# Performance work log

Hardware: AMD Instinct MI355X
Metric: run time of the kernel (lower is better)

## Reference

```python
import jax, jax.numpy as jnp
import numpy as np
from jax import lax

B, T, F = 4096, 100, 40
H_ENC, H_LAT, H_DEC = 64, 32, 64


def _lstm(x, Wih, Whh, b):
    """PyTorch-convention LSTM (gate order i,f,g,o), batch_first, zero init state.
    x: [B,T,Fin], Wih: [4H,Fin], Whh: [4H,H], b: [4H] (= b_ih + b_hh).
    Returns hidden sequence [B,T,H]."""
    H = Whh.shape[1]
    # precompute input contributions for all timesteps in one GEMM
    xg = jnp.einsum('btf,gf->btg', x, Wih) + b  # [B,T,4H]
    h0 = jnp.zeros((x.shape[0], H), dtype=x.dtype)
    c0 = jnp.zeros((x.shape[0], H), dtype=x.dtype)

    def step(carry, gx_t):
        h, c = carry
        gates = gx_t + h @ Whh.T  # [B,4H]
        i, f, g, o = jnp.split(gates, 4, axis=-1)
        c = jax.nn.sigmoid(f) * c + jax.nn.sigmoid(i) * jnp.tanh(g)
        h = jax.nn.sigmoid(o) * jnp.tanh(c)
        return (h, c), h

    _, hs = lax.scan(step, (h0, c0), jnp.swapaxes(xg, 0, 1))  # [T,B,H]
    return jnp.swapaxes(hs, 0, 1)


def setup_inputs() -> dict:
    key = jax.random.key(0)
    ks = jax.random.split(key, 8)
    s = 0.05
    return {
        'x': jax.random.normal(ks[0], (B, T, F), dtype=jnp.float32),
        'enc_Wih': jax.random.normal(ks[1], (4 * H_ENC, F), dtype=jnp.float32) * s,
        'enc_Whh': jax.random.normal(ks[2], (4 * H_ENC, H_ENC), dtype=jnp.float32) * s,
        'enc_b': jnp.zeros((4 * H_ENC,), dtype=jnp.float32),
        'lat_Wih': jax.random.normal(ks[3], (4 * H_LAT, H_ENC), dtype=jnp.float32) * s,
        'lat_Whh': jax.random.normal(ks[4], (4 * H_LAT, H_LAT), dtype=jnp.float32) * s,
        'lat_b': jnp.zeros((4 * H_LAT,), dtype=jnp.float32),
        'dec_Wih': jax.random.normal(ks[5], (4 * H_DEC, H_LAT), dtype=jnp.float32) * s,
        'dec_Whh': jax.random.normal(ks[6], (4 * H_DEC, H_DEC), dtype=jnp.float32) * s,
        'dec_b': jnp.zeros((4 * H_DEC,), dtype=jnp.float32),
        'out_W': jax.random.normal(ks[7], (F, H_DEC), dtype=jnp.float32) * s,
        'out_b': jnp.zeros((F,), dtype=jnp.float32),
    }


def reference(x, enc_Wih, enc_Whh, enc_b, lat_Wih, lat_Whh, lat_b,
              dec_Wih, dec_Whh, dec_b, out_W, out_b):
    h = _lstm(x, enc_Wih, enc_Whh, enc_b)                 # [B,T,64]
    last = h[:, -1:, :]                                   # [B,1,64]
    rep = jnp.broadcast_to(last, (h.shape[0], h.shape[1], last.shape[-1]))
    h = _lstm(rep, lat_Wih, lat_Whh, lat_b)               # [B,T,32]
    h = _lstm(h, dec_Wih, dec_Whh, dec_b)                 # [B,T,64]
    return jnp.einsum('bth,fh->btf', h, out_W) + out_b    # [B,T,40]
```

## Files before the change

kernel.cpp:

```cpp
#include <hip/hip_runtime.h>
#include <cstddef>

typedef __attribute__((ext_vector_type(8))) short bf16x8;
typedef __attribute__((ext_vector_type(4))) float f32x4;

#define MFMA(a, b, c) __builtin_amdgcn_mfma_f32_16x16x32_bf16((a), (b), (c), 0, 0, 0)

static __device__ __forceinline__ unsigned hi_bits(float f) {
  unsigned u = __builtin_bit_cast(unsigned, f);
  return (u + 0x8000u) & 0xFFFF0000u;
}
static __device__ __forceinline__ float asf(unsigned u) {
  return __builtin_bit_cast(float, u);
}
static __device__ __forceinline__ unsigned pack_hi(unsigned a, unsigned b) {
  return __builtin_amdgcn_perm(b, a, 0x07060302u);
}
static __device__ __forceinline__ unsigned short f2bf(float f) {
  unsigned u = __builtin_bit_cast(unsigned, f);
  u = u + 0x7FFFu + ((u >> 16) & 1u);
  return (unsigned short)(u >> 16);
}
static __device__ __forceinline__ float bf2f(unsigned short h) {
  unsigned u = ((unsigned)h) << 16;
  return __builtin_bit_cast(float, u);
}
static __device__ __forceinline__ float fast_sig(float x) {
  return __builtin_amdgcn_rcpf(1.0f + __expf(-x));
}
static __device__ __forceinline__ float fast_tanh(float x) {
  return 2.0f * __builtin_amdgcn_rcpf(1.0f + __expf(-2.0f * x)) - 1.0f;
}

static __device__ __forceinline__ void lds_barrier() {
  asm volatile("s_waitcnt lgkmcnt(0)\n\ts_barrier" ::: "memory");
}

static __device__ __forceinline__ bf16x8 aread(const char* base, int lane, int kc) {
  int b = lane & 15, g = lane >> 4;
  int off = (kc * 64 + g * 16) ^ ((b & 7) << 4);
  return *(const bf16x8*)(base + b * 256 + off);
}
static __device__ __forceinline__ void awrite16(char* base, int b, int k, unsigned short v) {
  int off = (2 * k) ^ ((b & 7) << 4);
  *(unsigned short*)(base + b * 256 + off) = v;
}
static __device__ __forceinline__ void awrite32(char* base, int b, int k, unsigned v) {
  int off = (2 * k) ^ ((b & 7) << 4);
  *(unsigned*)(base + b * 256 + off) = v;
}

extern "C" __global__ __launch_bounds__(512, 2)
void lstm_ae_mfma7(const float* __restrict__ x,
                   const float* __restrict__ eWih, const float* __restrict__ eWhh, const float* __restrict__ eb,
                   const float* __restrict__ lWih, const float* __restrict__ lWhh, const float* __restrict__ lb,
                   const float* __restrict__ dWih, const float* __restrict__ dWhh, const float* __restrict__ db,
                   const float* __restrict__ oW,  const float* __restrict__ ob,
                   float* __restrict__ out)
{
  __shared__ __align__(16) char sAhi[2][4096];
  __shared__ __align__(16) char sAlo[2][4096];

  const int tid  = threadIdx.x;
  const int lane = tid & 63;
  const int w    = tid >> 6;
  const int c16  = lane & 15;
  const int p4   = lane >> 4;
  const int bbase = blockIdx.x * 16;

  {
    f32x4 z = {0.f, 0.f, 0.f, 0.f};
    *(f32x4*)(&sAhi[0][0] + tid * 16) = z;
    *(f32x4*)(&sAlo[0][0] + tid * 16) = z;
  }

  bf16x8 ewh[2][4], ewl[2][4];
  float ebias[2][4];
#pragma unroll
  for (int n = 0; n < 2; ++n) {
    int tr = c16;
    int u = w * 8 + (tr >> 2) * 2 + n;
    int ga = tr & 3;
#pragma unroll
    for (int r = 0; r < 4; ++r) ebias[n][r] = eb[r * 64 + (w * 8 + p4 * 2 + n)];
#pragma unroll
    for (int kc = 0; kc < 4; ++kc) {
      bf16x8 hi, lo;
#pragma unroll
      for (int e = 0; e < 8; ++e) {
        int k = kc * 32 + p4 * 8 + e;
        float v = 0.f;
        if (k < 40)       v = eWih[(ga * 64 + u) * 40 + k];
        else if (k >= 64) v = eWhh[(ga * 64 + u) * 64 + (k - 64)];
        unsigned short hh = f2bf(v);
        hi[e] = (short)hh;
        lo[e] = (short)f2bf(v - bf2f(hh));
      }
      ewh[n][kc] = hi; ewl[n][kc] = lo;
    }
  }

  lds_barrier();

  if (tid < 160) {
    int b = tid / 10, f4 = tid - b * 10;
    f32x4 ld = *(const f32x4*)(x + ((size_t)(bbase + b) * 100 + 0) * 40 + f4 * 4);
    unsigned xh[4], xl[4];
#pragma unroll
    for (int e = 0; e < 4; ++e) {
      xh[e] = hi_bits(ld[e]);
      xl[e] = __builtin_bit_cast(unsigned, ld[e] - asf(xh[e]));
    }
    unsigned long long ph = (unsigned long long)pack_hi(xh[0], xh[1])
                          | ((unsigned long long)pack_hi(xh[2], xh[3]) << 32);
    unsigned long long pl = (unsigned long long)pack_hi(xl[0], xl[1])
                          | ((unsigned long long)pack_hi(xl[2], xl[3]) << 32);
    int off = (f4 * 8) ^ ((b & 7) << 4);
    *(unsigned long long*)(sAhi[0] + b * 256 + off) = ph;
    *(unsigned long long*)(sAlo[0] + b * 256 + off) = pl;
  }

  float cE[2] = {0.f, 0.f};
  int q = 0;
  lds_barrier();

#pragma unroll 1
  for (int t = 0; t < 100; ++t) {
    f32x4 xld;
    int sb = 0, sf4 = 0;
    const bool stager = (tid < 160);
    if (stager) {
      int tn = (t + 1 < 100) ? t + 1 : 99;
      sb = tid / 10; sf4 = tid - sb * 10;
      xld = *(const f32x4*)(x + ((size_t)(bbase + sb) * 100 + tn) * 40 + sf4 * 4);
    }

    f32x4 acc[2], acc2[2];
#pragma unroll
    for (int n = 0; n < 2; ++n) {
      acc[n]  = f32x4{ebias[n][0], ebias[n][1], ebias[n][2], ebias[n][3]};
      acc2[n] = f32x4{0.f, 0.f, 0.f, 0.f};
    }
    const char* Ah = sAhi[q];
    const char* Al = sAlo[q];
    __builtin_amdgcn_s_setprio(1);
#pragma unroll
    for (int kc = 0; kc < 4; ++kc) {
      bf16x8 ah = aread(Ah, lane, kc);
      bf16x8 al = aread(Al, lane, kc);
#pragma unroll
      for (int n = 0; n < 2; ++n) {
        f32x4 t0 = (kc < 2) ? acc[n] : acc2[n];
        t0 = MFMA(ewh[n][kc], ah, t0);
        t0 = MFMA(ewl[n][kc], ah, t0);
        t0 = MFMA(ewh[n][kc], al, t0);
        if (kc < 2) acc[n] = t0; else acc2[n] = t0;
      }
    }
    __builtin_amdgcn_s_setprio(0);

    char* AhN = sAhi[q ^ 1];
    char* AlN = sAlo[q ^ 1];
    unsigned hhb[2], hlb[2];
#pragma unroll
    for (int n = 0; n < 2; ++n) {
      f32x4 gv = acc[n] + acc2[n];
      float ii = fast_sig(gv[0]), ff = fast_sig(gv[1]);
      float gg = fast_tanh(gv[2]), oo = fast_sig(gv[3]);
      cE[n] = ff * cE[n] + ii * gg;
      float hv = oo * fast_tanh(cE[n]);
      hhb[n] = hi_bits(hv);
      hlb[n] = __builtin_bit_cast(unsigned, hv - asf(hhb[n]));
    }
    awrite32(AhN, c16, 64 + w * 8 + p4 * 2, pack_hi(hhb[0], hhb[1]));
    awrite32(AlN, c16, 64 + w * 8 + p4 * 2, pack_hi(hlb[0], hlb[1]));

    if (stager) {
      unsigned xh[4], xl[4];
#pragma unroll
      for (int e = 0; e < 4; ++e) {
        xh[e] = hi_bits(xld[e]);
        xl[e] = __builtin_bit_cast(unsigned, xld[e] - asf(xh[e]));
      }
      unsigned long long ph = (unsigned long long)pack_hi(xh[0], xh[1])
                            | ((unsigned long long)pack_hi(xh[2], xh[3]) << 32);
      unsigned long long pl = (unsigned long long)pack_hi(xl[0], xl[1])
                            | ((unsigned long long)pack_hi(xl[2], xl[3]) << 32);
      int off = (sf4 * 8) ^ ((sb & 7) << 4);
      *(unsigned long long*)(AhN + sb * 256 + off) = ph;
      *(unsigned long long*)(AlN + sb * 256 + off) = pl;
    }
    lds_barrier();
    q ^= 1;
  }

  f32x4 xga;
  {
    int tr = c16;
    int u = w * 4 + (tr >> 2), ga = tr & 3;
    int ul = w * 4 + p4;
    xga = f32x4{lb[ul], lb[32 + ul], lb[64 + ul], lb[96 + ul]};
#pragma unroll
    for (int kci = 0; kci < 2; ++kci) {
      bf16x8 hi, lo;
#pragma unroll
      for (int e = 0; e < 8; ++e) {
        float v = lWih[(ga * 32 + u) * 64 + kci * 32 + p4 * 8 + e];
        unsigned short hh = f2bf(v);
        hi[e] = (short)hh;
        lo[e] = (short)f2bf(v - bf2f(hh));
      }
      bf16x8 ah = aread(sAhi[q], lane, 2 + kci);
      bf16x8 al = aread(sAlo[q], lane, 2 + kci);
      xga = MFMA(hi, ah, xga);
      xga = MFMA(lo, ah, xga);
      xga = MFMA(hi, al, xga);
    }
  }
  lds_barrier();

  {
    f32x4 z = {0.f, 0.f, 0.f, 0.f};
    *(f32x4*)(&sAhi[0][0] + tid * 16) = z;
    *(f32x4*)(&sAlo[0][0] + tid * 16) = z;
  }

  bf16x8 lwh, lwl;
  {
    int tr = c16;
    int u = w * 4 + (tr >> 2), ga = tr & 3;
    bf16x8 hi, lo;
#pragma unroll
    for (int e = 0; e < 8; ++e) {
      float v = lWhh[(ga * 32 + u) * 32 + p4 * 8 + e];
      unsigned short hh = f2bf(v);
      hi[e] = (short)hh;
      lo[e] = (short)f2bf(v - bf2f(hh));
    }
    lwh = hi; lwl = lo;
  }
  bf16x8 dwh[2][3], dwl[2][3];
  float dbias[2][4];
#pragma unroll
  for (int n = 0; n < 2; ++n) {
    int tr = c16;
    int u = w * 8 + (tr >> 2) * 2 + n;
    int ga = tr & 3;
#pragma unroll
    for (int r = 0; r < 4; ++r) dbias[n][r] = db[r * 64 + (w * 8 + p4 * 2 + n)];
#pragma unroll
    for (int kc = 0; kc < 3; ++kc) {
      bf16x8 hi, lo;
#pragma unroll
      for (int e = 0; e < 8; ++e) {
        int k = kc * 32 + p4 * 8 + e;
        float v = (k < 32) ? dWih[(ga * 64 + u) * 32 + k]
                           : dWhh[(ga * 64 + u) * 64 + (k - 32)];
        unsigned short hh = f2bf(v);
        hi[e] = (short)hh;
        lo[e] = (short)f2bf(v - bf2f(hh));
      }
      dwh[n][kc] = hi; dwl[n][kc] = lo;
    }
  }
  bf16x8 pwh[2], pwl[2];
  float pbias[4];
#pragma unroll
  for (int r = 0; r < 4; ++r) {
    int f = w * 16 + p4 * 4 + r;
    pbias[r] = (w < 3 && f < 40) ? ob[f] : 0.0f;
  }
  if (w < 3) {
    int f = w * 16 + c16;
#pragma unroll
    for (int kci = 0; kci < 2; ++kci) {
      bf16x8 hi, lo;
#pragma unroll
      for (int e = 0; e < 8; ++e) {
        float v = (f < 40) ? oW[f * 64 + kci * 32 + p4 * 8 + e] : 0.0f;
        unsigned short hh = f2bf(v);
        hi[e] = (short)hh;
        lo[e] = (short)f2bf(v - bf2f(hh));
      }
      pwh[kci] = hi; pwl[kci] = lo;
    }
  }

  float cL = 0.f;
  float cD[2] = {0.f, 0.f};
  lds_barrier();

#pragma unroll 1
  for (int i = 0; i < 102; ++i) {
    const int pa = i & 1;
    bf16x8 c0h = aread(sAhi[pa ^ 1], lane, 0), c0l = aread(sAlo[pa ^ 1], lane, 0);
    bf16x8 d1h = aread(sAhi[pa], lane, 1),     d1l = aread(sAlo[pa], lane, 1);
    bf16x8 d2h = aread(sAhi[pa], lane, 2),     d2l = aread(sAlo[pa], lane, 2);

    if (i < 100) {
      __builtin_amdgcn_s_setprio(1);
      f32x4 lac = xga;
      lac = MFMA(lwh, c0h, lac);
      lac = MFMA(lwl, c0h, lac);
      lac = MFMA(lwh, c0l, lac);
      __builtin_amdgcn_s_setprio(0);
      float ii = fast_sig(lac[0]), ff = fast_sig(lac[1]);
      float gg = fast_tanh(lac[2]), oo = fast_sig(lac[3]);
      cL = ff * cL + ii * gg;
      float hv = oo * fast_tanh(cL);
      unsigned hb = hi_bits(hv);
      float lov = hv - asf(hb);
      awrite16(sAhi[pa], c16, w * 4 + p4, (unsigned short)(hb >> 16));
      awrite16(sAlo[pa], c16, w * 4 + p4,
               (unsigned short)(__builtin_bit_cast(unsigned, lov) >> 16));
    }

    if (i >= 1 && i < 101) {
      unsigned hhb[2], hlb[2];
#pragma unroll
      for (int n = 0; n < 2; ++n) {
        f32x4 dac = f32x4{dbias[n][0], dbias[n][1], dbias[n][2], dbias[n][3]};
        __builtin_amdgcn_s_setprio(1);
        dac = MFMA(dwh[n][0], c0h, dac);
        dac = MFMA(dwl[n][0], c0h, dac);
        dac = MFMA(dwh[n][0], c0l, dac);
        dac = MFMA(dwh[n][1], d1h, dac);
        dac = MFMA(dwl[n][1], d1h, dac);
        dac = MFMA(dwh[n][1], d1l, dac);
        dac = MFMA(dwh[n][2], d2h, dac);
        dac = MFMA(dwl[n][2], d2h, dac);
        dac = MFMA(dwh[n][2], d2l, dac);
        __builtin_amdgcn_s_setprio(0);
        float ii = fast_sig(dac[0]), ff = fast_sig(dac[1]);
        float gg = fast_tanh(dac[2]), oo = fast_sig(dac[3]);
        cD[n] = ff * cD[n] + ii * gg;
        float hv = oo * fast_tanh(cD[n]);
        hhb[n] = hi_bits(hv);
        hlb[n] = __builtin_bit_cast(unsigned, hv - asf(hhb[n]));
      }
      awrite32(sAhi[pa ^ 1], c16, 32 + w * 8 + p4 * 2, pack_hi(hhb[0], hhb[1]));
      awrite32(sAlo[pa ^ 1], c16, 32 + w * 8 + p4 * 2, pack_hi(hlb[0], hlb[1]));
    }

    if (i >= 2 && w < 3) {
      f32x4 pac = f32x4{pbias[0], pbias[1], pbias[2], pbias[3]};
      __builtin_amdgcn_s_setprio(1);
      pac = MFMA(pwh[0], d1h, pac);
      pac = MFMA(pwl[0], d1h, pac);
      pac = MFMA(pwh[0], d1l, pac);
      pac = MFMA(pwh[1], d2h, pac);
      pac = MFMA(pwl[1], d2h, pac);
      pac = MFMA(pwh[1], d2l, pac);
      __builtin_amdgcn_s_setprio(0);
#pragma unroll
      for (int r = 0; r < 4; ++r) {
        int f = w * 16 + p4 * 4 + r;
        if (f < 40)
          out[((size_t)(bbase + c16) * 100 + (i - 2)) * 40 + f] = pac[r];
      }
    }
    lds_barrier();
  }
}

extern "C" void kernel_launch(void* const* d_in, const int* in_sizes, int n_in,
                              void* d_out, int out_size, void* d_ws, size_t ws_size,
                              hipStream_t stream) {
  const float* x    = (const float*)d_in[0];
  const float* eWih = (const float*)d_in[1];
  const float* eWhh = (const float*)d_in[2];
  const float* eb   = (const float*)d_in[3];
  const float* lWih = (const float*)d_in[4];
  const float* lWhh = (const float*)d_in[5];
  const float* lb   = (const float*)d_in[6];
  const float* dWih = (const float*)d_in[7];
  const float* dWhh = (const float*)d_in[8];
  const float* db   = (const float*)d_in[9];
  const float* oW   = (const float*)d_in[10];
  const float* ob   = (const float*)d_in[11];
  float* out = (float*)d_out;

  lstm_ae_mfma7<<<256, 512, 0, stream>>>(x, eWih, eWhh, eb, lWih, lWhh, lb,
                                         dWih, dWhh, db, oW, ob, out);
}
```

Measured before the change: 186.9 us.

## Halve the batch tile per block to four waves and double units per wave

Each block now handles 8 batch rows with 256 threads instead of 16 rows with 512 threads, and the grid doubles to 512 blocks. Each wave computes twice as many gate units per step, so hidden-state writes become 64-bit LDS stores, and the split accumulators and setprio hints are dropped. The aim is smaller barrier groups and two independent blocks per CU that can hide each other's recurrence latency. The cost is that half of each 16-wide MFMA batch dimension now goes unused, which doubles MFMA work per batch row, and each wave's serial dependency chain per step gets longer.

```diff
diff --git a/kernel.cpp b/kernel.cpp
--- a/kernel.cpp
+++ b/kernel.cpp
@@ -41,17 +41,17 @@
   int off = (kc * 64 + g * 16) ^ ((b & 7) << 4);
   return *(const bf16x8*)(base + b * 256 + off);
 }
-static __device__ __forceinline__ void awrite16(char* base, int b, int k, unsigned short v) {
-  int off = (2 * k) ^ ((b & 7) << 4);
-  *(unsigned short*)(base + b * 256 + off) = v;
-}
 static __device__ __forceinline__ void awrite32(char* base, int b, int k, unsigned v) {
   int off = (2 * k) ^ ((b & 7) << 4);
   *(unsigned*)(base + b * 256 + off) = v;
 }
-
-extern "C" __global__ __launch_bounds__(512, 2)
-void lstm_ae_mfma7(const float* __restrict__ x,
+static __device__ __forceinline__ void awrite64(char* base, int b, int k, unsigned long long v) {
+  int off = (2 * k) ^ ((b & 7) << 4);
+  *(unsigned long long*)(base + b * 256 + off) = v;
+}
+
+extern "C" __global__ __launch_bounds__(256, 2)
+void lstm_ae_mfma8(const float* __restrict__ x,
                    const float* __restrict__ eWih, const float* __restrict__ eWhh, const float* __restrict__ eb,
                    const float* __restrict__ lWih, const float* __restrict__ lWhh, const float* __restrict__ lb,
                    const float* __restrict__ dWih, const float* __restrict__ dWhh, const float* __restrict__ db,
@@ -66,23 +66,25 @@
   const int w    = tid >> 6;
   const int c16  = lane & 15;
   const int p4   = lane >> 4;
-  const int bbase = blockIdx.x * 16;
+  const int bbase = blockIdx.x * 8;
 
   {
     f32x4 z = {0.f, 0.f, 0.f, 0.f};
-    *(f32x4*)(&sAhi[0][0] + tid * 16) = z;
-    *(f32x4*)(&sAlo[0][0] + tid * 16) = z;
-  }
-
-  bf16x8 ewh[2][4], ewl[2][4];
-  float ebias[2][4];
-#pragma unroll
-  for (int n = 0; n < 2; ++n) {
-    int tr = c16;
-    int u = w * 8 + (tr >> 2) * 2 + n;
-    int ga = tr & 3;
-#pragma unroll
-    for (int r = 0; r < 4; ++r) ebias[n][r] = eb[r * 64 + (w * 8 + p4 * 2 + n)];
+#pragma unroll
+    for (int i = 0; i < 2; ++i) {
+      *(f32x4*)(&sAhi[0][0] + tid * 16 + i * 4096) = z;
+      *(f32x4*)(&sAlo[0][0] + tid * 16 + i * 4096) = z;
+    }
+  }
+
+  bf16x8 ewh[4][4], ewl[4][4];
+  float ebias[4][4];
+#pragma unroll
+  for (int n = 0; n < 4; ++n) {
+    int u = w * 16 + (c16 >> 2) * 4 + n;
+    int ga = c16 & 3;
+#pragma unroll
+    for (int r = 0; r < 4; ++r) ebias[n][r] = eb[r * 64 + (w * 16 + p4 * 4 + n)];
 #pragma unroll
     for (int kc = 0; kc < 4; ++kc) {
       bf16x8 hi, lo;
@@ -102,9 +104,11 @@
 
   lds_barrier();
 
-  if (tid < 160) {
-    int b = tid / 10, f4 = tid - b * 10;
-    f32x4 ld = *(const f32x4*)(x + ((size_t)(bbase + b) * 100 + 0) * 40 + f4 * 4);
+  const bool stager = (tid >= 176);
+  const int s0 = tid - 176;
+  const int sb = s0 / 10, sf4 = s0 - (s0 / 10) * 10;
+  if (stager) {
+    f32x4 ld = *(const f32x4*)(x + ((size_t)(bbase + sb) * 100 + 0) * 40 + sf4 * 4);
     unsigned xh[4], xl[4];
 #pragma unroll
     for (int e = 0; e < 4; ++e) {
@@ -115,65 +119,61 @@
                           | ((unsigned long long)pack_hi(xh[2], xh[3]) << 32);
     unsigned long long pl = (unsigned long long)pack_hi(xl[0], xl[1])
                           | ((unsigned long long)pack_hi(xl[2], xl[3]) << 32);
-    int off = (f4 * 8) ^ ((b & 7) << 4);
-    *(unsigned long long*)(sAhi[0] + b * 256 + off) = ph;
-    *(unsigned long long*)(sAlo[0] + b * 256 + off) = pl;
-  }
-
-  float cE[2] = {0.f, 0.f};
+    int off = (sf4 * 8) ^ ((sb & 7) << 4);
+    *(unsigned long long*)(sAhi[0] + sb * 256 + off) = ph;
+    *(unsigned long long*)(sAlo[0] + sb * 256 + off) = pl;
+  }
+
+  float cE[4] = {0.f, 0.f, 0.f, 0.f};
   int q = 0;
   lds_barrier();
 
 #pragma unroll 1
   for (int t = 0; t < 100; ++t) {
     f32x4 xld;
-    int sb = 0, sf4 = 0;
-    const bool stager = (tid < 160);
     if (stager) {
       int tn = (t + 1 < 100) ? t + 1 : 99;
-      sb = tid / 10; sf4 = tid - sb * 10;
       xld = *(const f32x4*)(x + ((size_t)(bbase + sb) * 100 + tn) * 40 + sf4 * 4);
     }
 
-    f32x4 acc[2], acc2[2];
-#pragma unroll
-    for (int n = 0; n < 2; ++n) {
-      acc[n]  = f32x4{ebias[n][0], ebias[n][1], ebias[n][2], ebias[n][3]};
-      acc2[n] = f32x4{0.f, 0.f, 0.f, 0.f};
-    }
+    f32x4 acc[4];
+#pragma unroll
+    for (int n = 0; n < 4; ++n)
+      acc[n] = f32x4{ebias[n][0], ebias[n][1], ebias[n][2], ebias[n][3]};
     const char* Ah = sAhi[q];
     const char* Al = sAlo[q];
-    __builtin_amdgcn_s_setprio(1);
 #pragma unroll
     for (int kc = 0; kc < 4; ++kc) {
       bf16x8 ah = aread(Ah, lane, kc);
       bf16x8 al = aread(Al, lane, kc);
 #pragma unroll
-      for (int n = 0; n < 2; ++n) {
-        f32x4 t0 = (kc < 2) ? acc[n] : acc2[n];
-        t0 = MFMA(ewh[n][kc], ah, t0);
-        t0 = MFMA(ewl[n][kc], ah, t0);
-        t0 = MFMA(ewh[n][kc], al, t0);
-        if (kc < 2) acc[n] = t0; else acc2[n] = t0;
-      }
-    }
-    __builtin_amdgcn_s_setprio(0);
+      for (int n = 0; n < 4; ++n) {
+        acc[n] = MFMA(ewh[n][kc], ah, acc[n]);
+        acc[n] = MFMA(ewl[n][kc], ah, acc[n]);
+        acc[n] = MFMA(ewh[n][kc], al, acc[n]);
+      }
+    }
 
     char* AhN = sAhi[q ^ 1];
     char* AlN = sAlo[q ^ 1];
-    unsigned hhb[2], hlb[2];
-#pragma unroll
-    for (int n = 0; n < 2; ++n) {
-      f32x4 gv = acc[n] + acc2[n];
-      float ii = fast_sig(gv[0]), ff = fast_sig(gv[1]);
-      float gg = fast_tanh(gv[2]), oo = fast_sig(gv[3]);
+    unsigned hhb[4], hlb[4];
+#pragma unroll
+    for (int n = 0; n < 4; ++n) {
+      float ii = fast_sig(acc[n][0]), ff = fast_sig(acc[n][1]);
+      float gg = fast_tanh(acc[n][2]), oo = fast_sig(acc[n][3]);
       cE[n] = ff * cE[n] + ii * gg;
       float hv = oo * fast_tanh(cE[n]);
       hhb[n] = hi_bits(hv);
       hlb[n] = __builtin_bit_cast(unsigned, hv - asf(hhb[n]));
     }
-    awrite32(AhN, c16, 64 + w * 8 + p4 * 2, pack_hi(hhb[0], hhb[1]));
-    awrite32(AlN, c16, 64 + w * 8 + p4 * 2, pack_hi(hlb[0], hlb[1]));
+    {
+      unsigned long long ph = (unsigned long long)pack_hi(hhb[0], hhb[1])
+                            | ((unsigned long long)pack_hi(hhb[2], hhb[3]) << 32);
+      unsigned long long pl = (unsigned long long)pack_hi(hlb[0], hlb[1])
+                            | ((unsigned long long)pack_hi(hlb[2], hlb[3]) << 32);
+      awrite64(AhN, c16, 64 + w * 16 + p4 * 4, ph);
+      awrite64(AlN, c16, 64 + w * 16 + p4 * 4, pl);
+    }
 
     if (stager) {
       unsigned xh[4], xl[4];
@@ -194,41 +194,48 @@
     q ^= 1;
   }
 
-  f32x4 xga;
+  f32x4 xga[2];
   {
-    int tr = c16;
-    int u = w * 4 + (tr >> 2), ga = tr & 3;
-    int ul = w * 4 + p4;
-    xga = f32x4{lb[ul], lb[32 + ul], lb[64 + ul], lb[96 + ul]};
-#pragma unroll
-    for (int kci = 0; kci < 2; ++kci) {
-      bf16x8 hi, lo;
-#pragma unroll
-      for (int e = 0; e < 8; ++e) {
-        float v = lWih[(ga * 32 + u) * 64 + kci * 32 + p4 * 8 + e];
-        unsigned short hh = f2bf(v);
-        hi[e] = (short)hh;
-        lo[e] = (short)f2bf(v - bf2f(hh));
-      }
-      bf16x8 ah = aread(sAhi[q], lane, 2 + kci);
-      bf16x8 al = aread(sAlo[q], lane, 2 + kci);
-      xga = MFMA(hi, ah, xga);
-      xga = MFMA(lo, ah, xga);
-      xga = MFMA(hi, al, xga);
+#pragma unroll
+    for (int n = 0; n < 2; ++n) {
+      int u = w * 8 + (c16 >> 2) * 2 + n;
+      int ga = c16 & 3;
+      int ul = w * 8 + p4 * 2 + n;
+      xga[n] = f32x4{lb[ul], lb[32 + ul], lb[64 + ul], lb[96 + ul]};
+#pragma unroll
+      for (int kci = 0; kci < 2; ++kci) {
+        bf16x8 hi, lo;
+#pragma unroll
+        for (int e = 0; e < 8; ++e) {
+          float v = lWih[(ga * 32 + u) * 64 + kci * 32 + p4 * 8 + e];
+          unsigned short hh = f2bf(v);
+          hi[e] = (short)hh;
+          lo[e] = (short)f2bf(v - bf2f(hh));
+        }
+        bf16x8 ah = aread(sAhi[q], lane, 2 + kci);
+        bf16x8 al = aread(sAlo[q], lane, 2 + kci);
+        xga[n] = MFMA(hi, ah, xga[n]);
+        xga[n] = MFMA(lo, ah, xga[n]);
+        xga[n] = MFMA(hi, al, xga[n]);
+      }
     }
   }
   lds_barrier();
 
   {
     f32x4 z = {0.f, 0.f, 0.f, 0.f};
-    *(f32x4*)(&sAhi[0][0] + tid * 16) = z;
-    *(f32x4*)(&sAlo[0][0] + tid * 16) = z;
-  }
-
-  bf16x8 lwh, lwl;
-  {
-    int tr = c16;
-    int u = w * 4 + (tr >> 2), ga = tr & 3;
+#pragma unroll
+    for (int i = 0; i < 2; ++i) {
+      *(f32x4*)(&sAhi[0][0] + tid * 16 + i * 4096) = z;
+      *(f32x4*)(&sAlo[0][0] + tid * 16 + i * 4096) = z;
+    }
+  }
+
+  bf16x8 lwh[2], lwl[2];
+#pragma unroll
+  for (int n = 0; n < 2; ++n) {
+    int u = w * 8 + (c16 >> 2) * 2 + n;
+    int ga = c16 & 3;
     bf16x8 hi, lo;
 #pragma unroll
     for (int e = 0; e < 8; ++e) {
@@ -237,17 +244,16 @@
       hi[e] = (short)hh;
       lo[e] = (short)f2bf(v - bf2f(hh));
     }
-    lwh = hi; lwl = lo;
-  }
-  bf16x8 dwh[2][3], dwl[2][3];
-  float dbias[2][4];
-#pragma unroll
-  for (int n = 0; n < 2; ++n) {
-    int tr = c16;
-    int u = w * 8 + (tr >> 2) * 2 + n;
-    int ga = tr & 3;
-#pragma unroll
-    for (int r = 0; r < 4; ++r) dbias[n][r] = db[r * 64 + (w * 8 + p4 * 2 + n)];
+    lwh[n] = hi; lwl[n] = lo;
+  }
+  bf16x8 dwh[4][3], dwl[4][3];
+  float dbias[4][4];
+#pragma unroll
+  for (int n = 0; n < 4; ++n) {
+    int u = w * 16 + (c16 >> 2) * 4 + n;
+    int ga = c16 & 3;
+#pragma unroll
+    for (int r = 0; r < 4; ++r) dbias[n][r] = db[r * 64 + (w * 16 + p4 * 4 + n)];
 #pragma unroll
     for (int kc = 0; kc < 3; ++kc) {
       bf16x8 hi, lo;
@@ -286,8 +292,8 @@
     }
   }
 
-  float cL = 0.f;
-  float cD[2] = {0.f, 0.f};
+  float cL[2] = {0.f, 0.f};
+  float cD[4] = {0.f, 0.f, 0.f, 0.f};
   lds_barrier();
 
 #pragma unroll 1
@@ -298,29 +304,29 @@
     bf16x8 d2h = aread(sAhi[pa], lane, 2),     d2l = aread(sAlo[pa], lane, 2);
 
     if (i < 100) {
-      __builtin_amdgcn_s_setprio(1);
-      f32x4 lac = xga;
-      lac = MFMA(lwh, c0h, lac);
-      lac = MFMA(lwl, c0h, lac);
-      lac = MFMA(lwh, c0l, lac);
-      __builtin_amdgcn_s_setprio(0);
-      float ii = fast_sig(lac[0]), ff = fast_sig(lac[1]);
-      float gg = fast_tanh(lac[2]), oo = fast_sig(lac[3]);
-      cL = ff * cL + ii * gg;
-      float hv = oo * fast_tanh(cL);
-      unsigned hb = hi_bits(hv);
-      float lov = hv - asf(hb);
-      awrite16(sAhi[pa], c16, w * 4 + p4, (unsigned short)(hb >> 16));
-      awrite16(sAlo[pa], c16, w * 4 + p4,
-               (unsigned short)(__builtin_bit_cast(unsigned, lov) >> 16));
+      unsigned hb[2], lbits[2];
+#pragma unroll
+      for (int n = 0; n < 2; ++n) {
+        f32x4 lac = xga[n];
+        lac = MFMA(lwh[n], c0h, lac);
+        lac = MFMA(lwl[n], c0h, lac);
+        lac = MFMA(lwh[n], c0l, lac);
+        float ii = fast_sig(lac[0]), ff = fast_sig(lac[1]);
+        float gg = fast_tanh(lac[2]), oo = fast_sig(lac[3]);
+        cL[n] = ff * cL[n] + ii * gg;
+        float hv = oo * fast_tanh(cL[n]);
+        hb[n] = hi_bits(hv);
+        lbits[n] = __builtin_bit_cast(unsigned, hv - asf(hb[n]));
+      }
+      awrite32(sAhi[pa], c16, w * 8 + p4 * 2, pack_hi(hb[0], hb[1]));
+      awrite32(sAlo[pa], c16, w * 8 + p4 * 2, pack_hi(lbits[0], lbits[1]));
     }
 
     if (i >= 1 && i < 101) {
-      unsigned hhb[2], hlb[2];
-#pragma unroll
-      for (int n = 0; n < 2; ++n) {
+      unsigned hhb[4], hlb[4];
+#pragma unroll
+      for (int n = 0; n < 4; ++n) {
         f32x4 dac = f32x4{dbias[n][0], dbias[n][1], dbias[n][2], dbias[n][3]};
-        __builtin_amdgcn_s_setprio(1);
         dac = MFMA(dwh[n][0], c0h, dac);
         dac = MFMA(dwl[n][0], c0h, dac);
         dac = MFMA(dwh[n][0], c0l, dac);
@@ -330,7 +336,6 @@
         dac = MFMA(dwh[n][2], d2h, dac);
         dac = MFMA(dwl[n][2], d2h, dac);
         dac = MFMA(dwh[n][2], d2l, dac);
-        __builtin_amdgcn_s_setprio(0);
         float ii = fast_sig(dac[0]), ff = fast_sig(dac[1]);
         float gg = fast_tanh(dac[2]), oo = fast_sig(dac[3]);
         cD[n] = ff * cD[n] + ii * gg;
@@ -338,25 +343,29 @@
         hhb[n] = hi_bits(hv);
         hlb[n] = __builtin_bit_cast(unsigned, hv - asf(hhb[n]));
       }
-      awrite32(sAhi[pa ^ 1], c16, 32 + w * 8 + p4 * 2, pack_hi(hhb[0], hhb[1]));
-      awrite32(sAlo[pa ^ 1], c16, 32 + w * 8 + p4 * 2, pack_hi(hlb[0], hlb[1]));
+      unsigned long long ph = (unsigned long long)pack_hi(hhb[0], hhb[1])
+                            | ((unsigned long long)pack_hi(hhb[2], hhb[3]) << 32);
+      unsigned long long pl = (unsigned long long)pack_hi(hlb[0], hlb[1])
+                            | ((unsigned long long)pack_hi(hlb[2], hlb[3]) << 32);
+      awrite64(sAhi[pa ^ 1], c16, 32 + w * 16 + p4 * 4, ph);
+      awrite64(sAlo[pa ^ 1], c16, 32 + w * 16 + p4 * 4, pl);
     }
 
     if (i >= 2 && w < 3) {
       f32x4 pac = f32x4{pbias[0], pbias[1], pbias[2], pbias[3]};
-      __builtin_amdgcn_s_setprio(1);
       pac = MFMA(pwh[0], d1h, pac);
       pac = MFMA(pwl[0], d1h, pac);
       pac = MFMA(pwh[0], d1l, pac);
       pac = MFMA(pwh[1], d2h, pac);
       pac = MFMA(pwl[1], d2h, pac);
       pac = MFMA(pwh[1], d2l, pac);
-      __builtin_amdgcn_s_setprio(0);
-#pragma unroll
-      for (int r = 0; r < 4; ++r) {
-        int f = w * 16 + p4 * 4 + r;
-        if (f < 40)
-          out[((size_t)(bbase + c16) * 100 + (i - 2)) * 40 + f] = pac[r];
+      if (c16 < 8) {
+#pragma unroll
+        for (int r = 0; r < 4; ++r) {
+          int f = w * 16 + p4 * 4 + r;
+          if (f < 40)
+            out[((size_t)(bbase + c16) * 100 + (i - 2)) * 40 + f] = pac[r];
+        }
       }
     }
     lds_barrier();
@@ -380,6 +389,6 @@
   const float* ob   = (const float*)d_in[11];
   float* out = (float*)d_out;
 
-  lstm_ae_mfma7<<<256, 512, 0, stream>>>(x, eWih, eWhh, eb, lWih, lWhh, lb,
+  lstm_ae_mfma8<<<512, 256, 0, stream>>>(x, eWih, eWhh, eb, lWih, lWhh, lb,
                                          dWih, dWhh, db, oW, ob, out);
 }
```

New measurement: 321.8 us. 72.2% more time.
